# Optimization experiments

Measured on AMD Instinct MI355X. Metric: run time of the kernel, lower is better.

## Reference

```python
import jax, jax.numpy as jnp
import numpy as np

LATENT_DIM = 512
NUM_EMBEDDINGS = 4096
COMMITMENT_COST = 0.25
N_TOKENS = 32768


def setup_inputs() -> dict:
    key = jax.random.key(0)
    k_z, k_e = jax.random.split(key)
    z = jax.random.normal(k_z, (N_TOKENS, LATENT_DIM), dtype=jnp.float32)
    # embedding.weight ~ U(-1/K, 1/K), matching the torch init
    emb = jax.random.uniform(
        k_e, (NUM_EMBEDDINGS, LATENT_DIM), dtype=jnp.float32,
        minval=-1.0 / NUM_EMBEDDINGS, maxval=1.0 / NUM_EMBEDDINGS)
    return {"z": z, "emb": emb}


def reference(z, emb):
    flat_z = z.reshape(-1, LATENT_DIM)  # [N, D]
    # squared L2 distances: ||z||^2 + ||e||^2 - 2 z.e^T  -> [N, K]
    distances = (
        jnp.sum(flat_z ** 2, axis=1, keepdims=True)
        + jnp.sum(emb ** 2, axis=1)
        - 2.0 * jnp.matmul(flat_z, emb.T)
    )
    encoding_indices = jnp.argmin(distances, axis=1)  # [N]
    quantized = emb[encoding_indices].reshape(z.shape)  # [N, D]

    q_latent_loss = jnp.mean((jax.lax.stop_gradient(quantized) - z) ** 2)
    commitment_loss = jnp.mean((quantized - jax.lax.stop_gradient(z)) ** 2)
    vq_loss = q_latent_loss + COMMITMENT_COST * commitment_loss

    # codebook usage perplexity (histogram instead of dense one-hot)
    n = flat_z.shape[0]
    counts = jnp.zeros((NUM_EMBEDDINGS,), jnp.float32).at[encoding_indices].add(1.0)
    avg_probs = counts / n
    perplexity = jnp.exp(-jnp.sum(avg_probs * jnp.log(avg_probs + 1e-10)))

    # straight-through estimator
    quantized_st = z + jax.lax.stop_gradient(quantized - z)
    return quantized_st, vq_loss, perplexity
```

## Files before the change

kernel.cpp:

```cpp
#include <hip/hip_runtime.h>

#define NTOK   32768
#define DIM    512
#define NCODE  4096
#define NELEM  (NTOK*DIM)
#define COMMIT 0.25
#define ESCALE 8192.0f
#define EINV   (1.0f/4096.0f)
#define KSCL   262144.0f
#define KOFF   65536.0f

#define OFF_Z8      0ULL
#define OFF_E8      16777216ULL
#define OFF_EN32    18874368ULL
#define OFF_ROWMIN  18890752ULL
#define OFF_COUNTS  19021824ULL
#define OFF_SSE     19038208ULL

typedef int   v8i  __attribute__((ext_vector_type(8)));
typedef float v16f __attribute__((ext_vector_type(16)));

#define GLOBAL_AS __attribute__((address_space(1)))
#define LDS_AS    __attribute__((address_space(3)))

__device__ __forceinline__ void gld16(const void* g, void* l) {
    __builtin_amdgcn_global_load_lds((const GLOBAL_AS unsigned int*)g,
                                     (LDS_AS unsigned int*)l, 16, 0, 0);
}

__global__ void conv_kernel(const float* __restrict__ z, const float* __restrict__ e,
                            unsigned* __restrict__ z8, unsigned* __restrict__ e8,
                            unsigned* __restrict__ counts, double* __restrict__ sse) {
    const int ZI = NELEM / 16;
    const int TI = ZI + (NCODE * DIM) / 16;
    int i = blockIdx.x * blockDim.x + threadIdx.x;
    if (i < NCODE) counts[i] = 0u;
    if (i < 256)   sse[i] = 0.0;
    if (i >= TI) return;
    const float4* src; unsigned* dst; int j; float sc;
    if (i < ZI) { src = (const float4*)z; dst = z8; j = i; sc = 1.0f; }
    else        { src = (const float4*)e; dst = e8; j = i - ZI; sc = ESCALE; }
    uint4 o;
#pragma unroll
    for (int q = 0; q < 4; q++) {
        float4 v = src[j * 4 + q];
        int r = 0;
        r = __builtin_amdgcn_cvt_pk_fp8_f32(v.x * sc, v.y * sc, r, false);
        r = __builtin_amdgcn_cvt_pk_fp8_f32(v.z * sc, v.w * sc, r, true);
        (&o.x)[q] = (unsigned)r;
    }
    ((uint4*)dst)[j] = o;
}

__global__ void enorm_kernel(const float* __restrict__ emb, float* __restrict__ en32) {
    int gw = (blockIdx.x * blockDim.x + threadIdx.x) >> 6;
    int lane = threadIdx.x & 63;
    if (gw >= NCODE) return;
    const float4* p = (const float4*)(emb + (size_t)gw * DIM);
    float4 a = p[lane * 2], b = p[lane * 2 + 1];
    double s = (double)a.x*a.x + (double)a.y*a.y + (double)a.z*a.z + (double)a.w*a.w
             + (double)b.x*b.x + (double)b.y*b.y + (double)b.z*b.z + (double)b.w*b.w;
    for (int off = 32; off; off >>= 1) s += __shfl_down(s, off);
    if (lane == 0) en32[gw] = (float)s;
}

__global__ __launch_bounds__(256, 2)
void score_pass(const unsigned char* __restrict__ z8, const unsigned char* __restrict__ e8,
                const float* __restrict__ en32,
                unsigned* __restrict__ rowmin) {
    __shared__ __align__(16) unsigned char sB0[64 * 512];
    __shared__ __align__(16) unsigned char sB1[64 * 512];
    __shared__ __align__(16) float sEn[NCODE];
    const int tid = threadIdx.x;
    const int row0 = blockIdx.x * 64;
    const int wv = tid >> 6, ln = tid & 63;
    const int wm = wv & 1;
    const int wn = wv >> 1;
    const int c = ln & 31, h = ln >> 5;

#pragma unroll
    for (int s = 0; s < 8; s++) {
        int q = wv * 8 + s;
        int r = 2 * q + h;
        unsigned g = (unsigned)((ln & 31) ^ (r & 31));
        gld16(z8 + (size_t)(row0 + r) * 512 + g * 16u, sB1 + q * 1024);
    }
#pragma unroll
    for (int s = 0; s < 4; s++) {
        int chunk = wv * 4 + s;
        gld16((const unsigned char*)en32 + chunk * 1024 + (unsigned)(ln * 16),
              (unsigned char*)sEn + chunk * 1024);
    }

    unsigned eoff[8];
#pragma unroll
    for (int s = 0; s < 8; s++) {
        int q = wv * 8 + s;
        int r = 2 * q + h;
        unsigned g = (unsigned)((ln & 31) ^ (r & 31));
        eoff[s] = (unsigned)(r * 512) + g * 16u;
    }

    __builtin_amdgcn_sched_barrier(0);

#pragma unroll
    for (int s = 0; s < 8; s++)
        gld16(e8 + eoff[s], sB0 + (wv * 8 + s) * 1024);

    asm volatile("s_waitcnt vmcnt(8)" ::: "memory");
    __builtin_amdgcn_s_barrier();

    const int mrow = (wm * 32 + c) * 512;
    const int nrow = (wn * 32 + c) * 512;
    v8i za[8];
#pragma unroll
    for (int kt = 0; kt < 8; kt++) {
        int G = kt * 4 + 2 * h;
        uint4 x0 = *(const uint4*)(sB1 + mrow + (((G    ) ^ c) * 16));
        uint4 x1 = *(const uint4*)(sB1 + mrow + (((G + 1) ^ c) * 16));
        za[kt] = (v8i){(int)x0.x, (int)x0.y, (int)x0.z, (int)x0.w,
                       (int)x1.x, (int)x1.y, (int)x1.z, (int)x1.w};
    }
    asm volatile("s_waitcnt lgkmcnt(0)" ::: "memory");
    __builtin_amdgcn_s_barrier();

#pragma unroll
    for (int s = 0; s < 8; s++)
        gld16(e8 + 32768 + eoff[s], sB1 + (wv * 8 + s) * 1024);

    unsigned runmin[16];
#pragma unroll
    for (int reg = 0; reg < 16; reg++) runmin[reg] = 0xFFFFFFFFu;

    for (int ct = 0; ct < 64; ct++) {
        if (ct == 63) asm volatile("s_waitcnt vmcnt(0)" ::: "memory");
        else          asm volatile("s_waitcnt vmcnt(8)" ::: "memory");
        __builtin_amdgcn_s_barrier();

        const unsigned char* sB = (ct & 1) ? sB1 : sB0;
        float en = sEn[ct * 64 + wn * 32 + c];
        v16f acc0 = (v16f)(0.0f), acc1 = (v16f)(0.0f);
#pragma unroll
        for (int kt = 0; kt < 8; kt++) {
            int G = kt * 4 + 2 * h;
            uint4 y0 = *(const uint4*)(sB + nrow + (((G    ) ^ c) * 16));
            uint4 y1 = *(const uint4*)(sB + nrow + (((G + 1) ^ c) * 16));
            v8i b = (v8i){(int)y0.x, (int)y0.y, (int)y0.z, (int)y0.w,
                          (int)y1.x, (int)y1.y, (int)y1.z, (int)y1.w};
            if (kt & 1)
                acc1 = __builtin_amdgcn_mfma_scale_f32_32x32x64_f8f6f4(
                    za[kt], b, acc1, 0, 0, 0, 0x7F, 0, 0x7F);
            else
                acc0 = __builtin_amdgcn_mfma_scale_f32_32x32x64_f8f6f4(
                    za[kt], b, acc0, 0, 0, 0, 0x7F, 0, 0x7F);
        }

        unsigned n = (unsigned)(ct * 64 + wn * 32 + c);
#pragma unroll
        for (int reg = 0; reg < 16; reg++) {
            float s = en - (acc0[reg] + acc1[reg]) * EINV;
            unsigned kq = (unsigned)fmaf(s, KSCL, KOFF);
            unsigned p = (kq << 12) | n;
            runmin[reg] = runmin[reg] < p ? runmin[reg] : p;
        }

        asm volatile("s_waitcnt lgkmcnt(0)" ::: "memory");
        __builtin_amdgcn_s_barrier();

        if (ct < 62) {
            unsigned char* sD = (ct & 1) ? sB1 : sB0;
            const unsigned char* ebase = e8 + (size_t)(ct + 2) * 32768;
#pragma unroll
            for (int s = 0; s < 8; s++)
                gld16(ebase + eoff[s], sD + (wv * 8 + s) * 1024);
        }
    }

    __syncthreads();
    unsigned* tmp = (unsigned*)sB0;
#pragma unroll
    for (int reg = 0; reg < 16; reg++) {
        unsigned v = runmin[reg];
#pragma unroll
        for (int off = 1; off < 32; off <<= 1) {
            unsigned o = (unsigned)__shfl_xor((int)v, off);
            v = v < o ? v : o;
        }
        if (c == 0) {
            int rr = (reg & 3) + 8 * (reg >> 2) + 4 * h;
            tmp[(wm * 2 + wn) * 32 + rr] = v;
        }
    }
    __syncthreads();
    if (tid < 64) {
        int wmb = tid >> 5, rr = tid & 31;
        unsigned v0 = tmp[(wmb * 2 + 0) * 32 + rr];
        unsigned v1 = tmp[(wmb * 2 + 1) * 32 + rr];
        rowmin[row0 + tid] = v0 < v1 ? v0 : v1;
    }
}

__global__ void gather_loss(const float* __restrict__ z, const float* __restrict__ emb,
                            const unsigned* __restrict__ rowmin,
                            float* __restrict__ out, double* __restrict__ sse,
                            unsigned* __restrict__ counts) {
    int i = blockIdx.x * blockDim.x + threadIdx.x;
    float4 zv = ((const float4*)z)[i];
    int row = i >> 7, col = i & 127;
    unsigned code = rowmin[row] & 0xFFFu;
    if (col == 0) atomicAdd(&counts[code], 1u);
    float4 q = ((const float4*)emb)[code * 128 + col];
    float4 dv = make_float4(q.x - zv.x, q.y - zv.y, q.z - zv.z, q.w - zv.w);
    float4 o  = make_float4(zv.x + dv.x, zv.y + dv.y, zv.z + dv.z, zv.w + dv.w);
    ((float4*)out)[i] = o;
    double loc = (double)dv.x*dv.x + (double)dv.y*dv.y + (double)dv.z*dv.z + (double)dv.w*dv.w;
    for (int off = 32; off; off >>= 1) loc += __shfl_down(loc, off);
    __shared__ double sw[4];
    if ((threadIdx.x & 63) == 0) sw[threadIdx.x >> 6] = loc;
    __syncthreads();
    if (threadIdx.x == 0)
        atomicAdd(&sse[blockIdx.x & 255], sw[0] + sw[1] + sw[2] + sw[3]);
}

__global__ void finalize(const unsigned* __restrict__ counts, const double* __restrict__ sse,
                         float* __restrict__ out) {
    __shared__ double sh[256], sv[256];
    double h = 0.0;
    for (int b = threadIdx.x; b < NCODE; b += 256) {
        double p = (double)counts[b] / (double)NTOK;
        h += p * log(p + 1e-10);
    }
    sh[threadIdx.x] = h;
    sv[threadIdx.x] = sse[threadIdx.x];
    __syncthreads();
    for (int off = 128; off > 0; off >>= 1) {
        if (threadIdx.x < off) {
            sh[threadIdx.x] += sh[threadIdx.x + off];
            sv[threadIdx.x] += sv[threadIdx.x + off];
        }
        __syncthreads();
    }
    if (threadIdx.x == 0) {
        out[NELEM]     = (float)((1.0 + COMMIT) * sv[0] / (double)NELEM);
        out[NELEM + 1] = (float)exp(-sh[0]);
    }
}

extern "C" void kernel_launch(void* const* d_in, const int* in_sizes, int n_in,
                              void* d_out, int out_size, void* d_ws, size_t ws_size,
                              hipStream_t stream) {
    const float* z   = (const float*)d_in[0];
    const float* emb = (const float*)d_in[1];
    float* out = (float*)d_out;
    char* ws = (char*)d_ws;

    unsigned* z8 = (unsigned*)(ws + OFF_Z8);
    unsigned* e8 = (unsigned*)(ws + OFF_E8);
    float*    en32 = (float*)(ws + OFF_EN32);
    unsigned* rowmin = (unsigned*)(ws + OFF_ROWMIN);
    unsigned* counts = (unsigned*)(ws + OFF_COUNTS);
    double*   sse    = (double*)(ws + OFF_SSE);

    conv_kernel<<<(NELEM/16 + (NCODE*DIM)/16 + 255) / 256, 256, 0, stream>>>(
        z, emb, z8, e8, counts, sse);
    enorm_kernel<<<(NCODE * 64) / 256, 256, 0, stream>>>(emb, en32);

    score_pass<<<NTOK / 64, 256, 0, stream>>>((const unsigned char*)z8,
                                              (const unsigned char*)e8, en32, rowmin);

    gather_loss<<<NELEM / 4 / 256, 256, 0, stream>>>(z, emb, rowmin, out, sse, counts);
    finalize<<<1, 256, 0, stream>>>(counts, sse, out);
}
```

Before: 227.8 us.

## Widen score tile to 128 codes per stage so each wave reuses B across two row blocks

The score kernel now stages 128 codebook rows per pipeline step (64 KB double-buffered, 128 KB LDS) instead of 64. Each wave holds A fragments for all 64 token rows and issues two MFMAs per B fragment, halving LDS B reads per MFMA and halving the number of barriers. The prefetch for the next stage is issued before the min-reduction epilogue so the epilogue overlaps the loads, and the distance key arithmetic is folded into a single fma. In exchange, occupancy drops to one block per CU and each thread keeps twice as many accumulators and running minima in registers.

```diff
diff --git a/kernel.cpp b/kernel.cpp
--- a/kernel.cpp
+++ b/kernel.cpp
@@ -64,17 +64,16 @@
     if (lane == 0) en32[gw] = (float)s;
 }
 
-__global__ __launch_bounds__(256, 2)
+__global__ __launch_bounds__(256, 1)
 void score_pass(const unsigned char* __restrict__ z8, const unsigned char* __restrict__ e8,
                 const float* __restrict__ en32,
                 unsigned* __restrict__ rowmin) {
-    __shared__ __align__(16) unsigned char sB0[64 * 512];
-    __shared__ __align__(16) unsigned char sB1[64 * 512];
+    __shared__ __align__(16) unsigned char sE[4 * 32768];
     __shared__ __align__(16) float sEn[NCODE];
     const int tid = threadIdx.x;
     const int row0 = blockIdx.x * 64;
     const int wv = tid >> 6, ln = tid & 63;
-    const int wm = wv & 1;
+    const int t  = wv & 1;
     const int wn = wv >> 1;
     const int c = ln & 31, h = ln >> 5;
 
@@ -82,8 +81,8 @@
     for (int s = 0; s < 8; s++) {
         int q = wv * 8 + s;
         int r = 2 * q + h;
-        unsigned g = (unsigned)((ln & 31) ^ (r & 31));
-        gld16(z8 + (size_t)(row0 + r) * 512 + g * 16u, sB1 + q * 1024);
+        unsigned g = (unsigned)(c ^ (r & 31));
+        gld16(z8 + (size_t)(row0 + r) * 512 + g * 16u, sE + 65536 + q * 1024);
     }
 #pragma unroll
     for (int s = 0; s < 4; s++) {
@@ -92,111 +91,133 @@
               (unsigned char*)sEn + chunk * 1024);
     }
 
-    unsigned eoff[8];
-#pragma unroll
-    for (int s = 0; s < 8; s++) {
-        int q = wv * 8 + s;
-        int r = 2 * q + h;
-        unsigned g = (unsigned)((ln & 31) ^ (r & 31));
-        eoff[s] = (unsigned)(r * 512) + g * 16u;
+    unsigned eoff[16];
+#pragma unroll
+    for (int s = 0; s < 16; s++) {
+        int q = wv * 16 + s;
+        int rr = 2 * q + h;
+        unsigned g = (unsigned)(c ^ (rr & 31));
+        eoff[s] = (unsigned)(rr * 512) + g * 16u;
     }
 
     __builtin_amdgcn_sched_barrier(0);
 
 #pragma unroll
-    for (int s = 0; s < 8; s++)
-        gld16(e8 + eoff[s], sB0 + (wv * 8 + s) * 1024);
-
-    asm volatile("s_waitcnt vmcnt(8)" ::: "memory");
+    for (int s = 0; s < 16; s++)
+        gld16(e8 + eoff[s], sE + (wv * 16 + s) * 1024);
+
+    asm volatile("s_waitcnt vmcnt(16)" ::: "memory");
     __builtin_amdgcn_s_barrier();
 
-    const int mrow = (wm * 32 + c) * 512;
     const int nrow = (wn * 32 + c) * 512;
-    v8i za[8];
-#pragma unroll
-    for (int kt = 0; kt < 8; kt++) {
-        int G = kt * 4 + 2 * h;
-        uint4 x0 = *(const uint4*)(sB1 + mrow + (((G    ) ^ c) * 16));
-        uint4 x1 = *(const uint4*)(sB1 + mrow + (((G + 1) ^ c) * 16));
-        za[kt] = (v8i){(int)x0.x, (int)x0.y, (int)x0.z, (int)x0.w,
-                       (int)x1.x, (int)x1.y, (int)x1.z, (int)x1.w};
+    v8i za[2][8];
+#pragma unroll
+    for (int m = 0; m < 2; m++) {
+        const int mbase = 65536 + (m * 32 + c) * 512;
+#pragma unroll
+        for (int kt = 0; kt < 8; kt++) {
+            int G = kt * 4 + 2 * h;
+            union { uint4 u[2]; v8i v; } av;
+            av.u[0] = *(const uint4*)(sE + mbase + (((G    ) ^ c) * 16));
+            av.u[1] = *(const uint4*)(sE + mbase + (((G + 1) ^ c) * 16));
+            za[m][kt] = av.v;
+        }
     }
     asm volatile("s_waitcnt lgkmcnt(0)" ::: "memory");
     __builtin_amdgcn_s_barrier();
 
 #pragma unroll
-    for (int s = 0; s < 8; s++)
-        gld16(e8 + 32768 + eoff[s], sB1 + (wv * 8 + s) * 1024);
-
-    unsigned runmin[16];
-#pragma unroll
-    for (int reg = 0; reg < 16; reg++) runmin[reg] = 0xFFFFFFFFu;
-
-    for (int ct = 0; ct < 64; ct++) {
-        if (ct == 63) asm volatile("s_waitcnt vmcnt(0)" ::: "memory");
-        else          asm volatile("s_waitcnt vmcnt(8)" ::: "memory");
+    for (int s = 0; s < 16; s++)
+        gld16(e8 + 65536 + eoff[s], sE + 65536 + (wv * 16 + s) * 1024);
+
+    unsigned runmin[2][16];
+#pragma unroll
+    for (int m = 0; m < 2; m++)
+#pragma unroll
+    for (int reg = 0; reg < 16; reg++) runmin[m][reg] = 0xFFFFFFFFu;
+
+    const unsigned char* myb0 = sE + t * 32768 + nrow;
+    const unsigned char* myb1 = sE + 65536 + t * 32768 + nrow;
+    const unsigned nbase = (unsigned)(t * 64 + wn * 32 + c);
+
+    for (int ct = 0; ct < 32; ct++) {
+        if (ct == 31) asm volatile("s_waitcnt vmcnt(0)" ::: "memory");
+        else          asm volatile("s_waitcnt vmcnt(16)" ::: "memory");
         __builtin_amdgcn_s_barrier();
 
-        const unsigned char* sB = (ct & 1) ? sB1 : sB0;
-        float en = sEn[ct * 64 + wn * 32 + c];
-        v16f acc0 = (v16f)(0.0f), acc1 = (v16f)(0.0f);
+        const unsigned char* sB = (ct & 1) ? myb1 : myb0;
+        float en = sEn[ct * 128 + nbase];
+        float pre = fmaf(en, KSCL, KOFF);
+        v16f a0 = (v16f)(0.0f), a1 = (v16f)(0.0f);
+        v16f b0 = (v16f)(0.0f), b1 = (v16f)(0.0f);
 #pragma unroll
         for (int kt = 0; kt < 8; kt++) {
             int G = kt * 4 + 2 * h;
-            uint4 y0 = *(const uint4*)(sB + nrow + (((G    ) ^ c) * 16));
-            uint4 y1 = *(const uint4*)(sB + nrow + (((G + 1) ^ c) * 16));
-            v8i b = (v8i){(int)y0.x, (int)y0.y, (int)y0.z, (int)y0.w,
-                          (int)y1.x, (int)y1.y, (int)y1.z, (int)y1.w};
-            if (kt & 1)
-                acc1 = __builtin_amdgcn_mfma_scale_f32_32x32x64_f8f6f4(
-                    za[kt], b, acc1, 0, 0, 0, 0x7F, 0, 0x7F);
-            else
-                acc0 = __builtin_amdgcn_mfma_scale_f32_32x32x64_f8f6f4(
-                    za[kt], b, acc0, 0, 0, 0, 0x7F, 0, 0x7F);
-        }
-
-        unsigned n = (unsigned)(ct * 64 + wn * 32 + c);
-#pragma unroll
-        for (int reg = 0; reg < 16; reg++) {
-            float s = en - (acc0[reg] + acc1[reg]) * EINV;
-            unsigned kq = (unsigned)fmaf(s, KSCL, KOFF);
-            unsigned p = (kq << 12) | n;
-            runmin[reg] = runmin[reg] < p ? runmin[reg] : p;
+            union { uint4 u[2]; v8i v; } bv;
+            bv.u[0] = *(const uint4*)(sB + (((G    ) ^ c) * 16));
+            bv.u[1] = *(const uint4*)(sB + (((G + 1) ^ c) * 16));
+            if (kt & 1) {
+                a1 = __builtin_amdgcn_mfma_scale_f32_32x32x64_f8f6f4(
+                    za[0][kt], bv.v, a1, 0, 0, 0, 0x7F, 0, 0x7F);
+                b1 = __builtin_amdgcn_mfma_scale_f32_32x32x64_f8f6f4(
+                    za[1][kt], bv.v, b1, 0, 0, 0, 0x7F, 0, 0x7F);
+            } else {
+                a0 = __builtin_amdgcn_mfma_scale_f32_32x32x64_f8f6f4(
+                    za[0][kt], bv.v, a0, 0, 0, 0, 0x7F, 0, 0x7F);
+                b0 = __builtin_amdgcn_mfma_scale_f32_32x32x64_f8f6f4(
+                    za[1][kt], bv.v, b0, 0, 0, 0, 0x7F, 0, 0x7F);
+            }
         }
 
         asm volatile("s_waitcnt lgkmcnt(0)" ::: "memory");
         __builtin_amdgcn_s_barrier();
 
-        if (ct < 62) {
-            unsigned char* sD = (ct & 1) ? sB1 : sB0;
-            const unsigned char* ebase = e8 + (size_t)(ct + 2) * 32768;
-#pragma unroll
-            for (int s = 0; s < 8; s++)
-                gld16(ebase + eoff[s], sD + (wv * 8 + s) * 1024);
-        }
-    }
-
-    __syncthreads();
-    unsigned* tmp = (unsigned*)sB0;
-#pragma unroll
-    for (int reg = 0; reg < 16; reg++) {
-        unsigned v = runmin[reg];
-#pragma unroll
-        for (int off = 1; off < 32; off <<= 1) {
-            unsigned o = (unsigned)__shfl_xor((int)v, off);
-            v = v < o ? v : o;
-        }
-        if (c == 0) {
-            int rr = (reg & 3) + 8 * (reg >> 2) + 4 * h;
-            tmp[(wm * 2 + wn) * 32 + rr] = v;
+        if (ct < 30) {
+            unsigned char* sD = sE + (ct & 1) * 65536;
+            const unsigned char* ebase = e8 + (size_t)(ct + 2) * 65536;
+#pragma unroll
+            for (int s = 0; s < 16; s++)
+                gld16(ebase + eoff[s], sD + (wv * 16 + s) * 1024);
+        }
+
+        unsigned n = nbase + (unsigned)ct * 128u;
+#pragma unroll
+        for (int reg = 0; reg < 16; reg++) {
+            float s0 = a0[reg] + a1[reg];
+            unsigned k0 = (unsigned)fmaf(s0, -64.0f, pre);
+            unsigned p0 = (k0 << 12) | n;
+            runmin[0][reg] = runmin[0][reg] < p0 ? runmin[0][reg] : p0;
+            float s1 = b0[reg] + b1[reg];
+            unsigned k1 = (unsigned)fmaf(s1, -64.0f, pre);
+            unsigned p1 = (k1 << 12) | n;
+            runmin[1][reg] = runmin[1][reg] < p1 ? runmin[1][reg] : p1;
+        }
+    }
+
+    __syncthreads();
+    unsigned* tmp = (unsigned*)sE;
+#pragma unroll
+    for (int m = 0; m < 2; m++) {
+#pragma unroll
+        for (int reg = 0; reg < 16; reg++) {
+            unsigned v = runmin[m][reg];
+#pragma unroll
+            for (int off = 1; off < 32; off <<= 1) {
+                unsigned o = (unsigned)__shfl_xor((int)v, off);
+                v = v < o ? v : o;
+            }
+            if (c == 0) {
+                int r = m * 32 + (reg & 3) + 8 * (reg >> 2) + 4 * h;
+                tmp[wv * 64 + r] = v;
+            }
         }
     }
     __syncthreads();
     if (tid < 64) {
-        int wmb = tid >> 5, rr = tid & 31;
-        unsigned v0 = tmp[(wmb * 2 + 0) * 32 + rr];
-        unsigned v1 = tmp[(wmb * 2 + 1) * 32 + rr];
-        rowmin[row0 + tid] = v0 < v1 ? v0 : v1;
+        unsigned v0 = tmp[tid], v1 = tmp[64 + tid];
+        unsigned v2 = tmp[128 + tid], v3 = tmp[192 + tid];
+        unsigned a = v0 < v1 ? v0 : v1, b = v2 < v3 ? v2 : v3;
+        rowmin[row0 + tid] = a < b ? a : b;
     }
 }
 
```

After: 254.5 us. 11.7% more time.

## Fuse codebook norms into conversion and gather/loss into scoring kernel

Applied to the files above, without the earlier changes.

Codebook row norms are now computed inside the fp8 conversion kernel using a 32-lane shuffle reduction, which removes the separate enorm launch. The gather, straight-through output and SSE/histogram accumulation move into the tail of score_pass, using the row argmins held in shared memory, so the rowmin round-trip and the gather_loss launch go away. This cuts two kernel launches and some global traffic. In exchange the memory-bound gather runs inside the compute-heavy scoring blocks, which may lengthen their tail.

```diff
diff --git a/kernel.cpp b/kernel.cpp
--- a/kernel.cpp
+++ b/kernel.cpp
@@ -30,44 +30,44 @@
 
 __global__ void conv_kernel(const float* __restrict__ z, const float* __restrict__ e,
                             unsigned* __restrict__ z8, unsigned* __restrict__ e8,
-                            unsigned* __restrict__ counts, double* __restrict__ sse) {
+                            unsigned* __restrict__ counts, double* __restrict__ sse,
+                            float* __restrict__ en32) {
     const int ZI = NELEM / 16;
     const int TI = ZI + (NCODE * DIM) / 16;
     int i = blockIdx.x * blockDim.x + threadIdx.x;
     if (i < NCODE) counts[i] = 0u;
     if (i < 256)   sse[i] = 0.0;
     if (i >= TI) return;
+    const bool isEmb = (i >= ZI);
     const float4* src; unsigned* dst; int j; float sc;
-    if (i < ZI) { src = (const float4*)z; dst = z8; j = i; sc = 1.0f; }
+    if (!isEmb) { src = (const float4*)z; dst = z8; j = i; sc = 1.0f; }
     else        { src = (const float4*)e; dst = e8; j = i - ZI; sc = ESCALE; }
     uint4 o;
+    double nrm = 0.0;
 #pragma unroll
     for (int q = 0; q < 4; q++) {
         float4 v = src[j * 4 + q];
+        if (isEmb)
+            nrm += (double)v.x*v.x + (double)v.y*v.y + (double)v.z*v.z + (double)v.w*v.w;
         int r = 0;
         r = __builtin_amdgcn_cvt_pk_fp8_f32(v.x * sc, v.y * sc, r, false);
         r = __builtin_amdgcn_cvt_pk_fp8_f32(v.z * sc, v.w * sc, r, true);
         (&o.x)[q] = (unsigned)r;
     }
     ((uint4*)dst)[j] = o;
-}
-
-__global__ void enorm_kernel(const float* __restrict__ emb, float* __restrict__ en32) {
-    int gw = (blockIdx.x * blockDim.x + threadIdx.x) >> 6;
-    int lane = threadIdx.x & 63;
-    if (gw >= NCODE) return;
-    const float4* p = (const float4*)(emb + (size_t)gw * DIM);
-    float4 a = p[lane * 2], b = p[lane * 2 + 1];
-    double s = (double)a.x*a.x + (double)a.y*a.y + (double)a.z*a.z + (double)a.w*a.w
-             + (double)b.x*b.x + (double)b.y*b.y + (double)b.z*b.z + (double)b.w*b.w;
-    for (int off = 32; off; off >>= 1) s += __shfl_down(s, off);
-    if (lane == 0) en32[gw] = (float)s;
+    if (isEmb) {
+#pragma unroll
+        for (int off = 16; off; off >>= 1) nrm += __shfl_xor(nrm, off);
+        if ((j & 31) == 0) en32[j >> 5] = (float)nrm;
+    }
 }
 
 __global__ __launch_bounds__(256, 2)
 void score_pass(const unsigned char* __restrict__ z8, const unsigned char* __restrict__ e8,
                 const float* __restrict__ en32,
-                unsigned* __restrict__ rowmin) {
+                const float* __restrict__ zf32, const float* __restrict__ embf,
+                float* __restrict__ out, double* __restrict__ sse,
+                unsigned* __restrict__ counts) {
     __shared__ __align__(16) unsigned char sB0[64 * 512];
     __shared__ __align__(16) unsigned char sB1[64 * 512];
     __shared__ __align__(16) float sEn[NCODE];
@@ -192,33 +192,37 @@
         }
     }
     __syncthreads();
+    unsigned* rmin = (unsigned*)sB1;
     if (tid < 64) {
         int wmb = tid >> 5, rr = tid & 31;
         unsigned v0 = tmp[(wmb * 2 + 0) * 32 + rr];
         unsigned v1 = tmp[(wmb * 2 + 1) * 32 + rr];
-        rowmin[row0 + tid] = v0 < v1 ? v0 : v1;
-    }
-}
-
-__global__ void gather_loss(const float* __restrict__ z, const float* __restrict__ emb,
-                            const unsigned* __restrict__ rowmin,
-                            float* __restrict__ out, double* __restrict__ sse,
-                            unsigned* __restrict__ counts) {
-    int i = blockIdx.x * blockDim.x + threadIdx.x;
-    float4 zv = ((const float4*)z)[i];
-    int row = i >> 7, col = i & 127;
-    unsigned code = rowmin[row] & 0xFFFu;
-    if (col == 0) atomicAdd(&counts[code], 1u);
-    float4 q = ((const float4*)emb)[code * 128 + col];
-    float4 dv = make_float4(q.x - zv.x, q.y - zv.y, q.z - zv.z, q.w - zv.w);
-    float4 o  = make_float4(zv.x + dv.x, zv.y + dv.y, zv.z + dv.z, zv.w + dv.w);
-    ((float4*)out)[i] = o;
-    double loc = (double)dv.x*dv.x + (double)dv.y*dv.y + (double)dv.z*dv.z + (double)dv.w*dv.w;
+        unsigned best = v0 < v1 ? v0 : v1;
+        rmin[tid] = best & 0xFFFu;
+        atomicAdd(&counts[best & 0xFFFu], 1u);
+    }
+    __syncthreads();
+
+    const float4* zf = (const float4*)(zf32 + (size_t)row0 * 512);
+    float4*       of = (float4*)(out + (size_t)row0 * 512);
+    const float4* ef = (const float4*)embf;
+    double loc = 0.0;
+#pragma unroll 4
+    for (int it = 0; it < 32; it++) {
+        int idx = tid + it * 256;
+        int row = idx >> 7, col = idx & 127;
+        unsigned code = rmin[row];
+        float4 zv = zf[idx];
+        float4 q  = ef[code * 128 + col];
+        float dx = q.x - zv.x, dy = q.y - zv.y, dz = q.z - zv.z, dw = q.w - zv.w;
+        of[idx] = make_float4(zv.x + dx, zv.y + dy, zv.z + dz, zv.w + dw);
+        loc += (double)dx*dx + (double)dy*dy + (double)dz*dz + (double)dw*dw;
+    }
     for (int off = 32; off; off >>= 1) loc += __shfl_down(loc, off);
-    __shared__ double sw[4];
-    if ((threadIdx.x & 63) == 0) sw[threadIdx.x >> 6] = loc;
-    __syncthreads();
-    if (threadIdx.x == 0)
+    double* sw = (double*)sEn;
+    if (ln == 0) sw[wv] = loc;
+    __syncthreads();
+    if (tid == 0)
         atomicAdd(&sse[blockIdx.x & 255], sw[0] + sw[1] + sw[2] + sw[3]);
 }
 
@@ -257,17 +261,15 @@
     unsigned* z8 = (unsigned*)(ws + OFF_Z8);
     unsigned* e8 = (unsigned*)(ws + OFF_E8);
     float*    en32 = (float*)(ws + OFF_EN32);
-    unsigned* rowmin = (unsigned*)(ws + OFF_ROWMIN);
     unsigned* counts = (unsigned*)(ws + OFF_COUNTS);
     double*   sse    = (double*)(ws + OFF_SSE);
 
     conv_kernel<<<(NELEM/16 + (NCODE*DIM)/16 + 255) / 256, 256, 0, stream>>>(
-        z, emb, z8, e8, counts, sse);
-    enorm_kernel<<<(NCODE * 64) / 256, 256, 0, stream>>>(emb, en32);
+        z, emb, z8, e8, counts, sse, en32);
 
     score_pass<<<NTOK / 64, 256, 0, stream>>>((const unsigned char*)z8,
-                                              (const unsigned char*)e8, en32, rowmin);
-
-    gather_loss<<<NELEM / 4 / 256, 256, 0, stream>>>(z, emb, rowmin, out, sse, counts);
+                                              (const unsigned char*)e8, en32,
+                                              z, emb, out, sse, counts);
+
     finalize<<<1, 256, 0, stream>>>(counts, sse, out);
 }
```

Result: faster. 217.1 us (-4.7%).
